# Kernel tuning notes

Measured on AMD Instinct MI355X. Metric: run time of the kernel, lower is better.

## Reference

```python
import jax, jax.numpy as jnp
import numpy as np

VOCAB = 32000
DIM = 1024
LAYERS = 4
B = 4
L = 1024


def setup_inputs() -> dict:
    key = jax.random.key(0)
    ks = jax.random.split(key, 5)
    input_ids = jax.random.randint(ks[0], (B, L), 0, VOCAB)
    embed = jax.random.normal(ks[1], (VOCAB, DIM), jnp.float32) * 0.02
    # 1/sqrt(fan_in) scaling keeps the recurrent state numerically stable over L steps
    W = jax.random.normal(ks[2], (LAYERS, 2 * DIM, 2 * DIM), jnp.float32) * (1.0 / np.sqrt(2 * DIM))
    out_w = jax.random.normal(ks[3], (VOCAB, DIM), jnp.float32) * 0.02
    starter = jax.random.normal(ks[4], (LAYERS, DIM), jnp.float32) * 0.02
    return {"input_ids": input_ids, "embed": embed, "W": W, "out_w": out_w, "starter": starter}


def reference(input_ids, embed, W, out_w, starter):
    Bsz, Lsz = input_ids.shape
    d = starter.shape[1]
    x = embed[input_ids]  # [B, L, d]
    # initial per-layer state, broadcast over batch: [layers, B, d]
    s0 = jnp.broadcast_to(starter[:, None, :], (W.shape[0], Bsz, d))

    def time_step(s_stack, x_t):
        # s_stack: [layers, B, d], x_t: [B, d]
        def layer_step(h, ws):
            Wi, si = ws  # Wi: [2d, 2d], si: [B, d]
            out = jnp.concatenate([h, si], axis=-1) @ Wi.T  # [B, 2d]
            h_new, s_new = jnp.split(out, 2, axis=-1)
            return h_new, s_new
        y, new_s = jax.lax.scan(layer_step, x_t, (W, s_stack))
        return new_s, y

    _, ys = jax.lax.scan(time_step, s0, jnp.swapaxes(x, 0, 1))  # ys: [L, B, d]
    logits = jnp.einsum('lbd,vd->blv', ys, out_w)  # [B, L, vocab]
    return logits
```

## Files before the change

kernel.cpp:

```cpp
#include <hip/hip_runtime.h>
#include <hip/hip_bf16.h>
#include <stdint.h>

#define BATCH 4
#define SEQ 1024
#define DIMX 1024
#define VOCAB 32000
#define NLAYERS 4
#define NBLK 256

#define W_GARR 4096
#define W_GREL 4608
#define W_LREL 4864
#define W_FLAG 5120

using bf16x8 = __attribute__((ext_vector_type(8))) short;
using f32x4v = __attribute__((ext_vector_type(4))) float;

__device__ __forceinline__ uint16_t f2b(float f) {
  __hip_bfloat16 h = __float2bfloat16(f);
  return *reinterpret_cast<uint16_t*>(&h);
}
__device__ __forceinline__ float b2f(uint16_t u) {
  __hip_bfloat16 h = *reinterpret_cast<__hip_bfloat16*>(&u);
  return __bfloat162float(h);
}
__device__ __forceinline__ void fsplit(float v, uint16_t& h, uint16_t& l) {
  h = f2b(v);
  l = f2b(v - b2f(h));
}

__device__ __forceinline__ uint32_t get_xcc() {
  uint32_t x;
  asm volatile("s_getreg_b32 %0, hwreg(HW_REG_XCC_ID)" : "=s"(x));
  return x & 7u;
}

__global__ __launch_bounds__(256) void k_embed_split(const int* __restrict__ ids,
                                                     const float* __restrict__ emb,
                                                     uint16_t* __restrict__ Hhi,
                                                     uint16_t* __restrict__ Hlo) {
  int idx = blockIdx.x * 256 + threadIdx.x;
  int d4 = idx & (DIMX / 4 - 1);
  int tb = idx >> 8;
  int t = tb >> 2, b = tb & 3;
  int id = ids[b * SEQ + t];
  float4 v = reinterpret_cast<const float4*>(emb + (size_t)id * DIMX)[d4];
  ushort4 h, l;
  fsplit(v.x, h.x, l.x); fsplit(v.y, h.y, l.y); fsplit(v.z, h.z, l.z); fsplit(v.w, h.w, l.w);
  reinterpret_cast<ushort4*>(Hhi)[idx] = h;
  reinterpret_cast<ushort4*>(Hlo)[idx] = l;
}

__global__ __launch_bounds__(256) void k_split_w(const float* __restrict__ W,
                                                 uint16_t* __restrict__ W1h, uint16_t* __restrict__ W1l,
                                                 uint16_t* __restrict__ WSh, uint16_t* __restrict__ WSl,
                                                 uint16_t* __restrict__ M1h, uint16_t* __restrict__ M1l) {
  int idx = blockIdx.x * 256 + threadIdx.x;
  int c4 = idx & 255;
  int row = idx >> 8;
  int l = row >> 12, r = row & 4095;
  const float* Wl = W + (size_t)l * 4 * 1024 * 1024;
  const float* src;
  uint16_t *dh, *dl;
  size_t doff;
  if (r < 2048) { src = Wl + (size_t)r * 2048; dh = W1h; dl = W1l; doff = ((size_t)l * 2048 + r) * 1024; }
  else if (r < 3072) { int rr = r - 2048; src = Wl + (size_t)rr * 2048 + 1024; dh = WSh; dl = WSl; doff = ((size_t)l * 1024 + rr) * 1024; }
  else { int rr = r - 3072; src = Wl + (size_t)(1024 + rr) * 2048 + 1024; dh = M1h; dl = M1l; doff = ((size_t)l * 1024 + rr) * 1024; }
  float4 v = reinterpret_cast<const float4*>(src)[c4];
  ushort4 h, lo4;
  fsplit(v.x, h.x, lo4.x); fsplit(v.y, h.y, lo4.y); fsplit(v.z, h.z, lo4.z); fsplit(v.w, h.w, lo4.w);
  reinterpret_cast<ushort4*>(dh + doff)[c4] = h;
  reinterpret_cast<ushort4*>(dl + doff)[c4] = lo4;
}

__global__ __launch_bounds__(256) void k_trans_w(const float* __restrict__ W,
                                                 uint16_t* __restrict__ T1h, uint16_t* __restrict__ T1l) {
  __shared__ float t[64][65];
  int l = blockIdx.z;
  const float* Wl = W + (size_t)l * 4 * 1024 * 1024;
  int i0 = blockIdx.y * 64, j0 = blockIdx.x * 64;
  int c4 = (threadIdx.x & 15) * 4, rr = threadIdx.x >> 4;
#pragma unroll
  for (int p = 0; p < 4; ++p) {
    int r = rr + p * 16;
    float4 v = *reinterpret_cast<const float4*>(Wl + (size_t)(1024 + i0 + r) * 2048 + 1024 + j0 + c4);
    t[r][c4] = v.x; t[r][c4 + 1] = v.y; t[r][c4 + 2] = v.z; t[r][c4 + 3] = v.w;
  }
  __syncthreads();
#pragma unroll
  for (int p = 0; p < 4; ++p) {
    int j = rr + p * 16;
    ushort4 h, l4;
    fsplit(t[c4 + 0][j], h.x, l4.x);
    fsplit(t[c4 + 1][j], h.y, l4.y);
    fsplit(t[c4 + 2][j], h.z, l4.z);
    fsplit(t[c4 + 3][j], h.w, l4.w);
    size_t o = (size_t)l * 1024 * 1024 + (size_t)(j0 + j) * 1024 + i0 + c4;
    *reinterpret_cast<ushort4*>(T1h + o) = h;
    *reinterpret_cast<ushort4*>(T1l + o) = l4;
  }
}

template <int BM, int BN>
__global__ __launch_bounds__(256) void k_mfma(
    int K,
    const uint16_t* __restrict__ Ahi, const uint16_t* __restrict__ Alo, int a_cs, int a_bs, size_t a_z,
    const uint16_t* __restrict__ Bhi, const uint16_t* __restrict__ Blo, int ldb, size_t b_z,
    const float* __restrict__ ADD, int add_cs, int add_bs,
    float* __restrict__ O1f, int o1_cs, int o1_bs,
    uint16_t* __restrict__ O1hi, uint16_t* __restrict__ O1lo, int o1s_cs, int o1s_bs, int split_n0, size_t o1_z,
    uint16_t* __restrict__ O2hi, uint16_t* __restrict__ O2lo, int o2_cs, int o2_bs, size_t o2_z) {
  constexpr int FM = BM / 32;
  constexpr int FN = BN / 32;
  __shared__ uint16_t sAh[BM * 32], sAl[BM * 32], sBh[BN * 32], sBl[BN * 32];
  size_t zb = blockIdx.z;
  Ahi += zb * a_z; Alo += zb * a_z;
  Bhi += zb * b_z; Blo += zb * b_z;
  if (O1hi) { O1hi += zb * o1_z; O1lo += zb * o1_z; }
  if (O2hi) { O2hi += zb * o2_z; O2lo += zb * o2_z; }
  int tid = threadIdx.x;
  int lane = tid & 63;
  int wave = tid >> 6;
  int wm = wave >> 1, wn = wave & 1;
  int m0 = blockIdx.y * BM, n0 = blockIdx.x * BN;
  f32x4v acc[FM][FN] = {};
  for (int kt = 0; kt < K; kt += 32) {
    __syncthreads();
#pragma unroll
    for (int q = 0; q < BM / 64; ++q) {
      int off = q * 4096 + tid * 16;
      int r = off >> 6;
      int cu = (off & 63) >> 1;
      size_t goff = (size_t)(m0 / 4 + (r >> 2)) * a_cs + (size_t)(r & 3) * a_bs + kt + cu;
      __builtin_amdgcn_global_load_lds(
          (const __attribute__((address_space(1))) uint32_t*)(Ahi + goff),
          (__attribute__((address_space(3))) uint32_t*)((char*)sAh + off), 16, 0, 0);
      __builtin_amdgcn_global_load_lds(
          (const __attribute__((address_space(1))) uint32_t*)(Alo + goff),
          (__attribute__((address_space(3))) uint32_t*)((char*)sAl + off), 16, 0, 0);
    }
#pragma unroll
    for (int q = 0; q < BN / 64; ++q) {
      int off = q * 4096 + tid * 16;
      int r = off >> 6, cu = (off & 63) >> 1;
      size_t goff = (size_t)(n0 + r) * ldb + kt + cu;
      __builtin_amdgcn_global_load_lds(
          (const __attribute__((address_space(1))) uint32_t*)(Bhi + goff),
          (__attribute__((address_space(3))) uint32_t*)((char*)sBh + off), 16, 0, 0);
      __builtin_amdgcn_global_load_lds(
          (const __attribute__((address_space(1))) uint32_t*)(Blo + goff),
          (__attribute__((address_space(3))) uint32_t*)((char*)sBl + off), 16, 0, 0);
    }
    __syncthreads();
    int rsel = lane & 15, ko = (lane >> 4) * 8;
    bf16x8 ah[FM], al[FM], bh[FN], bl[FN];
#pragma unroll
    for (int mf = 0; mf < FM; ++mf) {
      int row = wm * (FM * 16) + mf * 16 + rsel;
      ah[mf] = *reinterpret_cast<const bf16x8*>(sAh + row * 32 + ko);
      al[mf] = *reinterpret_cast<const bf16x8*>(sAl + row * 32 + ko);
    }
#pragma unroll
    for (int nf = 0; nf < FN; ++nf) {
      int row = wn * (FN * 16) + nf * 16 + rsel;
      bh[nf] = *reinterpret_cast<const bf16x8*>(sBh + row * 32 + ko);
      bl[nf] = *reinterpret_cast<const bf16x8*>(sBl + row * 32 + ko);
    }
#pragma unroll
    for (int mf = 0; mf < FM; ++mf)
#pragma unroll
      for (int nf = 0; nf < FN; ++nf) {
        acc[mf][nf] = __builtin_amdgcn_mfma_f32_16x16x32_bf16(ah[mf], bh[nf], acc[mf][nf], 0, 0, 0);
        acc[mf][nf] = __builtin_amdgcn_mfma_f32_16x16x32_bf16(ah[mf], bl[nf], acc[mf][nf], 0, 0, 0);
        acc[mf][nf] = __builtin_amdgcn_mfma_f32_16x16x32_bf16(al[mf], bh[nf], acc[mf][nf], 0, 0, 0);
      }
  }
  int rowg = (lane >> 4) * 4, colg = lane & 15;
#pragma unroll
  for (int mf = 0; mf < FM; ++mf)
#pragma unroll
    for (int nf = 0; nf < FN; ++nf)
#pragma unroll
      for (int r = 0; r < 4; ++r) {
        int m = m0 + wm * (FM * 16) + mf * 16 + rowg + r;
        int n = n0 + wn * (FN * 16) + nf * 16 + colg;
        size_t ro = (size_t)(m >> 2);
        float dot = acc[mf][nf][r];
        float v = dot;
        if (ADD) v += ADD[ro * add_cs + (size_t)(m & 3) * add_bs + n];
        if (O1f) O1f[ro * o1_cs + (size_t)(m & 3) * o1_bs + n] = v;
        if (O1hi && n >= split_n0) {
          uint16_t h, l;
          fsplit(v, h, l);
          size_t o = ro * o1s_cs + (size_t)(m & 3) * o1s_bs + (n - split_n0);
          O1hi[o] = h; O1lo[o] = l;
        }
        if (O2hi) {
          uint16_t h, l;
          fsplit(dot, h, l);
          size_t o = (o2_bs == 0) ? ((size_t)n * o2_cs + m)
                                  : (ro * o2_cs + (size_t)(m & 3) * o2_bs + n);
          O2hi[o] = h; O2lo[o] = l;
        }
      }
}

__device__ __forceinline__ void bar_any(uint32_t* S, int flat, int global, uint32_t& gen) {
  gen++;
  __syncthreads();
  int bid = blockIdx.x, tid = threadIdx.x;
  if (flat) {
    if (tid == 0)
      __hip_atomic_store(S + (size_t)bid * 16, gen, __ATOMIC_RELEASE, __HIP_MEMORY_SCOPE_AGENT);
    if (bid == 0) {
      while (__hip_atomic_load(S + (size_t)tid * 16, __ATOMIC_RELAXED, __HIP_MEMORY_SCOPE_AGENT) < gen)
        __builtin_amdgcn_s_sleep(2);
      __syncthreads();
      if (tid == 0) {
        __builtin_amdgcn_fence(__ATOMIC_ACQUIRE, "agent");
        __hip_atomic_store(S + W_GREL, gen, __ATOMIC_RELEASE, __HIP_MEMORY_SCOPE_AGENT);
      }
      __syncthreads();
    } else {
      if (tid == 0) {
        while (__hip_atomic_load(S + W_GREL, __ATOMIC_RELAXED, __HIP_MEMORY_SCOPE_AGENT) < gen)
          __builtin_amdgcn_s_sleep(2);
        __builtin_amdgcn_fence(__ATOMIC_ACQUIRE, "agent");
      }
      __syncthreads();
    }
    return;
  }
  int xcd = bid & 7, q = bid >> 3;
  if (global) {
    if (q != 0) {
      if (tid == 0) {
        __hip_atomic_store(S + (size_t)(xcd * 32 + q) * 16, gen, __ATOMIC_RELAXED, __HIP_MEMORY_SCOPE_AGENT);
        while (__hip_atomic_load(S + W_LREL + xcd * 16, __ATOMIC_RELAXED, __HIP_MEMORY_SCOPE_AGENT) < gen)
          __builtin_amdgcn_s_sleep(1);
        asm volatile("buffer_inv sc0" ::: "memory");
      }
      __builtin_amdgcn_sched_barrier(0);
      __syncthreads();
    } else {
      if (tid < 31) {
        uint32_t* s = S + (size_t)(xcd * 32 + 1 + tid) * 16;
        while (__hip_atomic_load(s, __ATOMIC_RELAXED, __HIP_MEMORY_SCOPE_AGENT) < gen)
          __builtin_amdgcn_s_sleep(1);
      }
      __syncthreads();
      if (tid == 0)
        __hip_atomic_store(S + W_GARR + xcd * 16, gen, __ATOMIC_RELEASE, __HIP_MEMORY_SCOPE_AGENT);
      if (xcd == 0) {
        if (tid < 8) {
          while (__hip_atomic_load(S + W_GARR + tid * 16, __ATOMIC_RELAXED, __HIP_MEMORY_SCOPE_AGENT) < gen)
            __builtin_amdgcn_s_sleep(1);
        }
        __syncthreads();
        if (tid == 0)
          __hip_atomic_store(S + W_GREL, gen, __ATOMIC_RELEASE, __HIP_MEMORY_SCOPE_AGENT);
      }
      if (tid == 0) {
        while (__hip_atomic_load(S + W_GREL, __ATOMIC_RELAXED, __HIP_MEMORY_SCOPE_AGENT) < gen)
          __builtin_amdgcn_s_sleep(1);
        __builtin_amdgcn_fence(__ATOMIC_ACQUIRE, "agent");
        __hip_atomic_store(S + W_LREL + xcd * 16, gen, __ATOMIC_RELEASE, __HIP_MEMORY_SCOPE_AGENT);
      }
      __builtin_amdgcn_sched_barrier(0);
      __syncthreads();
    }
  } else {
    if (q != 0) {
      if (tid == 0) {
        __hip_atomic_store(S + (size_t)(xcd * 32 + q) * 16, gen, __ATOMIC_RELAXED, __HIP_MEMORY_SCOPE_AGENT);
        while (__hip_atomic_load(S + W_LREL + xcd * 16, __ATOMIC_RELAXED, __HIP_MEMORY_SCOPE_AGENT) < gen)
          __builtin_amdgcn_s_sleep(1);
        asm volatile("buffer_inv sc0" ::: "memory");
      }
      __builtin_amdgcn_sched_barrier(0);
      __syncthreads();
    } else {
      if (tid < 31) {
        uint32_t* s = S + (size_t)(xcd * 32 + 1 + tid) * 16;
        while (__hip_atomic_load(s, __ATOMIC_RELAXED, __HIP_MEMORY_SCOPE_AGENT) < gen)
          __builtin_amdgcn_s_sleep(1);
      }
      __syncthreads();
      if (tid == 0) {
        asm volatile("buffer_inv sc0" ::: "memory");
        __hip_atomic_store(S + W_LREL + xcd * 16, gen, __ATOMIC_RELAXED, __HIP_MEMORY_SCOPE_AGENT);
      }
      __builtin_amdgcn_sched_barrier(0);
      __syncthreads();
    }
  }
}

__device__ __forceinline__ f32x4v wtile16(
    const uint16_t* __restrict__ Ah, const uint16_t* __restrict__ Al,
    int a_cs, int a_bs, int m0,
    const uint16_t* __restrict__ Bh, const uint16_t* __restrict__ Bl,
    int n0, int lane) {
  int rsel = lane & 15, ko = (lane >> 4) * 8;
  int am = m0 + rsel;
  const uint16_t* pah = Ah + (size_t)(am >> 2) * a_cs + (size_t)(am & 3) * a_bs + ko;
  const uint16_t* pal = Al + (size_t)(am >> 2) * a_cs + (size_t)(am & 3) * a_bs + ko;
  const uint16_t* pbh = Bh + (size_t)(n0 + rsel) * 1024 + ko;
  const uint16_t* pbl = Bl + (size_t)(n0 + rsel) * 1024 + ko;
  f32x4v acc = {0.f, 0.f, 0.f, 0.f};
#pragma unroll 4
  for (int kt = 0; kt < 1024; kt += 32) {
    bf16x8 ah = *reinterpret_cast<const bf16x8*>(pah + kt);
    bf16x8 al = *reinterpret_cast<const bf16x8*>(pal + kt);
    bf16x8 bh = *reinterpret_cast<const bf16x8*>(pbh + kt);
    bf16x8 bl = *reinterpret_cast<const bf16x8*>(pbl + kt);
    acc = __builtin_amdgcn_mfma_f32_16x16x32_bf16(ah, bh, acc, 0, 0, 0);
    acc = __builtin_amdgcn_mfma_f32_16x16x32_bf16(ah, bl, acc, 0, 0, 0);
    acc = __builtin_amdgcn_mfma_f32_16x16x32_bf16(al, bh, acc, 0, 0, 0);
  }
  return acc;
}

__device__ __forceinline__ f32x4v wtile16_lds(
    const uint16_t* __restrict__ Ah, const uint16_t* __restrict__ Al,
    int a_cs, int a_bs, int m0,
    const uint16_t* sBh, const uint16_t* sBl,
    int lane) {
  int rsel = lane & 15, ko = (lane >> 4) * 8;
  int am = m0 + rsel;
  const uint16_t* pah = Ah + (size_t)(am >> 2) * a_cs + (size_t)(am & 3) * a_bs + ko;
  const uint16_t* pal = Al + (size_t)(am >> 2) * a_cs + (size_t)(am & 3) * a_bs + ko;
  int rb = rsel * 1024;
  int s7 = rsel & 7;
  f32x4v acc0 = {0.f, 0.f, 0.f, 0.f}, acc1 = {0.f, 0.f, 0.f, 0.f};
#pragma unroll 4
  for (int kt = 0; kt < 1024; kt += 64) {
    int e0 = kt + ko, e1 = kt + 32 + ko;
    int o0 = rb + ((((e0) >> 3) ^ s7) << 3);
    int o1 = rb + ((((e1) >> 3) ^ s7) << 3);
    bf16x8 ah0 = *reinterpret_cast<const bf16x8*>(pah + kt);
    bf16x8 al0 = *reinterpret_cast<const bf16x8*>(pal + kt);
    bf16x8 ah1 = *reinterpret_cast<const bf16x8*>(pah + kt + 32);
    bf16x8 al1 = *reinterpret_cast<const bf16x8*>(pal + kt + 32);
    bf16x8 bh0 = *reinterpret_cast<const bf16x8*>(sBh + o0);
    bf16x8 bl0 = *reinterpret_cast<const bf16x8*>(sBl + o0);
    bf16x8 bh1 = *reinterpret_cast<const bf16x8*>(sBh + o1);
    bf16x8 bl1 = *reinterpret_cast<const bf16x8*>(sBl + o1);
    acc0 = __builtin_amdgcn_mfma_f32_16x16x32_bf16(ah0, bh0, acc0, 0, 0, 0);
    acc1 = __builtin_amdgcn_mfma_f32_16x16x32_bf16(ah1, bh1, acc1, 0, 0, 0);
    acc0 = __builtin_amdgcn_mfma_f32_16x16x32_bf16(ah0, bl0, acc0, 0, 0, 0);
    acc1 = __builtin_amdgcn_mfma_f32_16x16x32_bf16(ah1, bl1, acc1, 0, 0, 0);
    acc0 = __builtin_amdgcn_mfma_f32_16x16x32_bf16(al0, bh0, acc0, 0, 0, 0);
    acc1 = __builtin_amdgcn_mfma_f32_16x16x32_bf16(al1, bh1, acc1, 0, 0, 0);
  }
  return acc0 + acc1;
}

__global__ __launch_bounds__(256) void k_layer(
    uint32_t* S,
    float* __restrict__ P,
    uint16_t* __restrict__ PUh, uint16_t* __restrict__ PUl,
    uint16_t* __restrict__ Sh, uint16_t* __restrict__ Sl,
    const uint16_t* __restrict__ M1h, const uint16_t* __restrict__ M1l,
    const uint16_t* __restrict__ M16h, const uint16_t* __restrict__ M16l,
    const uint16_t* __restrict__ M128h, const uint16_t* __restrict__ M128l,
    uint16_t* G3h0, uint16_t* G3l0, uint16_t* G3h1, uint16_t* G3l1,
    uint16_t* BEh, uint16_t* BEl,
    float* LAMf, uint16_t* LAMh, uint16_t* LAMl,
    uint16_t* GSh0, uint16_t* GSl0, uint16_t* GSh1, uint16_t* GSl1,
    const float* __restrict__ starterL) {
  __shared__ uint16_t sB[2][32 * 1024];
  int tid = threadIdx.x, bid = blockIdx.x;
  int lane = tid & 63;
  int wv = tid >> 6;
  int xcd = bid & 7;
  int q = bid >> 3;
  uint32_t gen = 0;
  int rowg = (lane >> 4) * 4, colg = lane & 15;

  int m0_13 = xcd * 32 + (wv & 1) * 16;
  int n0_13 = (2 * q + (wv >> 1)) * 16;
  int lrb13 = (wv >> 1) * 16 * 1024;
  int n0_2 = (q * 4 + wv) * 16;

  {
    int idx = bid * 256 + tid;
    if (idx < BATCH * DIMX) {
      int b = idx >> 10, d = idx & 1023;
      float v = starterL[d];
      uint16_t h, l;
      fsplit(v, h, l);
      size_t o = (size_t)b * 1024 + d;
      BEh[o] = h; BEl[o] = l;
      G3h0[o] = h; G3l0[o] = l;
      GSh0[o] = h; GSl0[o] = l;
      Sh[o] = h; Sl[o] = l;
    }
  }

  if (tid == 0 && get_xcc() != (uint32_t)xcd)
    __hip_atomic_store(S + W_FLAG, 1u, __ATOMIC_RELAXED, __HIP_MEMORY_SCOPE_AGENT);
  bar_any(S, 1, 1, gen);
  int flat = (int)__hip_atomic_load(S + W_FLAG, __ATOMIC_RELAXED, __HIP_MEMORY_SCOPE_AGENT);

  {
    const uint16_t* gh = M1h + (size_t)(32 * q) * 1024;
    const uint16_t* gl = M1l + (size_t)(32 * q) * 1024;
    for (int i = tid; i < 32 * 128; i += 256) {
      int r = i >> 7, c8 = i & 127;
      int dst = r * 1024 + ((c8 ^ (r & 7)) << 3);
      *reinterpret_cast<bf16x8*>(&sB[0][dst]) = *reinterpret_cast<const bf16x8*>(gh + (size_t)r * 1024 + c8 * 8);
      *reinterpret_cast<bf16x8*>(&sB[1][dst]) = *reinterpret_cast<const bf16x8*>(gl + (size_t)r * 1024 + c8 * 8);
    }
  }
  __syncthreads();

  for (int j = 1; j < 16; ++j) {
    {
      f32x4v acc = wtile16_lds(PUh + (size_t)(j - 1) * 4096, PUl + (size_t)(j - 1) * 4096,
                               65536, 1024, m0_13, &sB[0][lrb13], &sB[1][lrb13], lane);
      int n = n0_13 + colg;
#pragma unroll
      for (int rr = 0; rr < 4; ++rr) {
        int m = m0_13 + rowg + rr;
        int c = m >> 2, b = m & 3;
        size_t t = (size_t)(c * 16 + j);
        float* pu = P + (t * 4 + b) * 2048 + 1024 + n;
        float v = acc[rr] + *pu;
        *pu = v;
        uint16_t h, l;
        fsplit(v, h, l);
        size_t o = (t * 4 + b) * 1024 + n;
        PUh[o] = h; PUl[o] = l;
      }
    }
    bar_any(S, flat, 0, gen);
  }

  if (q == 0) {
    for (int i = tid; i < 4096; i += 256) {
      int b = i >> 10, d = i & 1023;
      float v = P[((size_t)(xcd * 128 + 15) * 4 + b) * 2048 + 1024 + d];
      size_t o = (size_t)xcd * 16384 + (size_t)b * 1024 + d;
      LAMf[o] = v;
      uint16_t h, l;
      fsplit(v, h, l);
      LAMh[o] = h; LAMl[o] = l;
    }
  }
  bar_any(S, flat, 0, gen);

  for (int j = 1; j < 8; ++j) {
    if (q < 16) {
      size_t abase = (size_t)(j - 1) * 131072 + (size_t)xcd * 16384;
      f32x4v acc = wtile16(LAMh + abase, LAMl + abase, 4096, 1024, 0, M16h, M16l, n0_2, lane);
      if (rowg == 0) {
        int n = n0_2 + colg;
#pragma unroll
        for (int rr = 0; rr < 4; ++rr) {
          int b = rr;
          int c = 8 * xcd + j;
          float e = P[((size_t)(c * 16 + 15) * 4 + b) * 2048 + 1024 + n];
          float v = acc[rr] + e;
          size_t o = (size_t)j * 131072 + (size_t)xcd * 16384 + (size_t)b * 1024 + n;
          LAMf[o] = v;
          uint16_t h, l;
          fsplit(v, h, l);
          LAMh[o] = h; LAMl[o] = l;
        }
      }
    }
    bar_any(S, flat, (j == 7) ? 1 : 0, gen);
  }

  for (int g = 0; g < 7; ++g) {
    if (xcd == 0 && q < 16) {
      f32x4v acc = wtile16(BEh + (size_t)g * 16384, BEl + (size_t)g * 16384,
                           4096, 1024, 0, M128h, M128l, n0_2, lane);
      if (rowg == 0) {
        int n = n0_2 + colg;
#pragma unroll
        for (int rr = 0; rr < 4; ++rr) {
          int b = rr;
          float v = acc[rr] + LAMf[(size_t)7 * 131072 + (size_t)g * 16384 + (size_t)b * 1024 + n];
          uint16_t h, l;
          fsplit(v, h, l);
          size_t ob = (size_t)(g + 1) * 16384 + (size_t)b * 1024 + n;
          BEh[ob] = h; BEl[ob] = l;
          int c = 8 * (g + 1);
          size_t o1 = (size_t)(c * 4 + b) * 1024 + n;
          G3h0[o1] = h; G3l0[o1] = l;
          size_t o2 = ((size_t)(c * 16) * 4 + b) * 1024 + n;
          Sh[o2] = h; Sl[o2] = l;
          GSh0[ob] = h; GSl0[ob] = l;
        }
      }
    }
    bar_any(S, flat, (g == 6) ? 1 : 0, gen);
  }

  int gsc = 0;
  for (int j = 1; j < 8; ++j) {
    uint16_t* gih = gsc ? GSh1 : GSh0;
    uint16_t* gil = gsc ? GSl1 : GSl0;
    uint16_t* goh = gsc ? GSh0 : GSh1;
    uint16_t* gol = gsc ? GSl0 : GSl1;
    if (q < 16) {
      size_t gbase = (size_t)xcd * 16384;
      f32x4v acc = wtile16(gih + gbase, gil + gbase, 4096, 1024, 0, M16h, M16l, n0_2, lane);
      if (rowg == 0) {
        int n = n0_2 + colg;
#pragma unroll
        for (int rr = 0; rr < 4; ++rr) {
          int b = rr;
          int c = 8 * xcd + j;
          float lam = LAMf[(size_t)(j - 1) * 131072 + (size_t)xcd * 16384 + (size_t)b * 1024 + n];
          float v = acc[rr] + lam;
          uint16_t h, l;
          fsplit(v, h, l);
          size_t o1 = (size_t)(c * 4 + b) * 1024 + n;
          G3h0[o1] = h; G3l0[o1] = l;
          size_t o2 = ((size_t)(c * 16) * 4 + b) * 1024 + n;
          Sh[o2] = h; Sl[o2] = l;
          uint16_t h2, l2;
          fsplit(acc[rr], h2, l2);
          goh[gbase + (size_t)b * 1024 + n] = h2;
          gol[gbase + (size_t)b * 1024 + n] = l2;
        }
      }
    }
    bar_any(S, flat, 0, gen);
    gsc ^= 1;
  }

  int g3 = 0;
  for (int j = 1; j < 16; ++j) {
    uint16_t* gih = g3 ? G3h1 : G3h0;
    uint16_t* gil = g3 ? G3l1 : G3l0;
    uint16_t* goh = g3 ? G3h0 : G3h1;
    uint16_t* gol = g3 ? G3l0 : G3l1;
    {
      f32x4v acc = wtile16_lds(gih, gil, 4096, 1024, m0_13, &sB[0][lrb13], &sB[1][lrb13], lane);
      int n = n0_13 + colg;
#pragma unroll
      for (int rr = 0; rr < 4; ++rr) {
        int m = m0_13 + rowg + rr;
        int c = m >> 2, b = m & 3;
        float u = P[((size_t)(c * 16 + j - 1) * 4 + b) * 2048 + 1024 + n];
        float v = acc[rr] + u;
        uint16_t h, l;
        fsplit(v, h, l);
        size_t o = ((size_t)(c * 16 + j) * 4 + b) * 1024 + n;
        Sh[o] = h; Sl[o] = l;
        uint16_t h2, l2;
        fsplit(acc[rr], h2, l2);
        goh[(size_t)m * 1024 + n] = h2;
        gol[(size_t)m * 1024 + n] = l2;
      }
    }
    if (j < 15) bar_any(S, flat, 0, gen);
    g3 ^= 1;
  }
}

__global__ __launch_bounds__(256) void k_reorder_hi(const uint16_t* __restrict__ Hhi, uint16_t* __restrict__ Y) {
  int idx = blockIdx.x * 256 + threadIdx.x;
  int d4 = idx & (DIMX / 4 - 1);
  int tb = idx >> 8;
  int t = tb >> 2, b = tb & 3;
  ushort4 v = reinterpret_cast<const ushort4*>(Hhi)[idx];
  reinterpret_cast<ushort4*>(Y + (size_t)(b * SEQ + t) * DIMX)[d4] = v;
}

__global__ __launch_bounds__(256) void k_cast_w(const float* __restrict__ src, uint16_t* __restrict__ dst, int n4) {
  int idx = blockIdx.x * 256 + threadIdx.x;
  if (idx >= n4) return;
  float4 v = reinterpret_cast<const float4*>(src)[idx];
  ushort4 o;
  o.x = f2b(v.x); o.y = f2b(v.y); o.z = f2b(v.z); o.w = f2b(v.w);
  reinterpret_cast<ushort4*>(dst)[idx] = o;
}

__global__ __launch_bounds__(256) void k_logits(const uint16_t* __restrict__ A,
                                                const uint16_t* __restrict__ Bt,
                                                float* __restrict__ C) {
  __shared__ uint16_t As[128 * 32];
  __shared__ uint16_t Bs[128 * 32];
  int tid = threadIdx.x;
  int bx = blockIdx.x, by = blockIdx.y;
  int lane = tid & 63, wave = tid >> 6;
  int wm = wave >> 1, wn = wave & 1;
  f32x4v acc[4][4] = {};
  const uint16_t* Ag = A + (size_t)by * 128 * 1024;
  const uint16_t* Bg = Bt + (size_t)bx * 128 * 1024;
  for (int kt = 0; kt < 1024; kt += 32) {
    __syncthreads();
#pragma unroll
    for (int q = 0; q < 2; ++q) {
      int off = q * 4096 + tid * 16;
      int r = off >> 6, cu = (off & 63) >> 1;
      __builtin_amdgcn_global_load_lds(
          (const __attribute__((address_space(1))) uint32_t*)(Ag + (size_t)r * 1024 + kt + cu),
          (__attribute__((address_space(3))) uint32_t*)((char*)As + off), 16, 0, 0);
      __builtin_amdgcn_global_load_lds(
          (const __attribute__((address_space(1))) uint32_t*)(Bg + (size_t)r * 1024 + kt + cu),
          (__attribute__((address_space(3))) uint32_t*)((char*)Bs + off), 16, 0, 0);
    }
    __syncthreads();
    int rsel = lane & 15, ko = (lane >> 4) * 8;
    bf16x8 af[4], bfr[4];
#pragma unroll
    for (int mf = 0; mf < 4; ++mf)
      af[mf] = *reinterpret_cast<const bf16x8*>(As + (wm * 64 + mf * 16 + rsel) * 32 + ko);
#pragma unroll
    for (int nf = 0; nf < 4; ++nf)
      bfr[nf] = *reinterpret_cast<const bf16x8*>(Bs + (wn * 64 + nf * 16 + rsel) * 32 + ko);
#pragma unroll
    for (int mf = 0; mf < 4; ++mf)
#pragma unroll
      for (int nf = 0; nf < 4; ++nf)
        acc[mf][nf] = __builtin_amdgcn_mfma_f32_16x16x32_bf16(af[mf], bfr[nf], acc[mf][nf], 0, 0, 0);
  }
  int rowg = (lane >> 4) * 4;
  int colg = lane & 15;
#pragma unroll
  for (int mf = 0; mf < 4; ++mf)
#pragma unroll
    for (int nf = 0; nf < 4; ++nf)
#pragma unroll
      for (int r = 0; r < 4; ++r) {
        int m = by * 128 + wm * 64 + mf * 16 + rowg + r;
        int n = bx * 128 + wn * 64 + nf * 16 + colg;
        C[(size_t)m * VOCAB + n] = acc[mf][nf][r];
      }
}

extern "C" void kernel_launch(void* const* d_in, const int* in_sizes, int n_in,
                              void* d_out, int out_size, void* d_ws, size_t ws_size,
                              hipStream_t stream) {
  const int* ids = (const int*)d_in[0];
  const float* emb = (const float*)d_in[1];
  const float* W = (const float*)d_in[2];
  const float* outw = (const float*)d_in[3];
  const float* starter = (const float*)d_in[4];
  float* out = (float*)d_out;

  char* wsb = (char*)d_ws;
  size_t off = 0;
  auto alloc = [&](size_t bytes) {
    void* p = wsb + off;
    off = (off + bytes + 255) & ~(size_t)255;
    return p;
  };
  const size_t TB = SEQ * BATCH;
  const size_t MB1 = (size_t)1024 * 1024;

  uint32_t* SYNC = (uint32_t*)alloc((size_t)NLAYERS * 8192 * 4);
  uint16_t* Hh[2] = {(uint16_t*)alloc(TB * DIMX * 2), (uint16_t*)alloc(TB * DIMX * 2)};
  uint16_t* Hl[2] = {(uint16_t*)alloc(TB * DIMX * 2), (uint16_t*)alloc(TB * DIMX * 2)};
  float* P = (float*)alloc(TB * 2 * DIMX * 4);
  uint16_t* PUh = (uint16_t*)alloc(TB * DIMX * 2);
  uint16_t* PUl = (uint16_t*)alloc(TB * DIMX * 2);
  uint16_t* Sh = (uint16_t*)alloc(TB * DIMX * 2);
  uint16_t* Sl = (uint16_t*)alloc(TB * DIMX * 2);
  uint16_t* W1h = (uint16_t*)alloc((size_t)NLAYERS * 2048 * 1024 * 2);
  uint16_t* W1l = (uint16_t*)alloc((size_t)NLAYERS * 2048 * 1024 * 2);
  uint16_t* WSh = (uint16_t*)alloc((size_t)NLAYERS * MB1 * 2);
  uint16_t* WSl = (uint16_t*)alloc((size_t)NLAYERS * MB1 * 2);
  uint16_t* M1h = (uint16_t*)alloc((size_t)NLAYERS * MB1 * 2);
  uint16_t* M1l = (uint16_t*)alloc((size_t)NLAYERS * MB1 * 2);
  uint16_t* T1h = (uint16_t*)alloc((size_t)NLAYERS * MB1 * 2);
  uint16_t* T1l = (uint16_t*)alloc((size_t)NLAYERS * MB1 * 2);
  uint16_t* M16Ah = (uint16_t*)alloc((size_t)NLAYERS * MB1 * 2);
  uint16_t* M16Al = (uint16_t*)alloc((size_t)NLAYERS * MB1 * 2);
  uint16_t* M128Ah = (uint16_t*)alloc((size_t)NLAYERS * MB1 * 2);
  uint16_t* M128Al = (uint16_t*)alloc((size_t)NLAYERS * MB1 * 2);
  uint16_t* G3h0 = (uint16_t*)alloc((size_t)256 * 1024 * 2);
  uint16_t* G3l0 = (uint16_t*)alloc((size_t)256 * 1024 * 2);
  uint16_t* G3h1 = (uint16_t*)alloc((size_t)256 * 1024 * 2);
  uint16_t* G3l1 = (uint16_t*)alloc((size_t)256 * 1024 * 2);
  uint16_t* BEh = (uint16_t*)alloc((size_t)8 * 16 * 1024 * 2);
  uint16_t* BEl = (uint16_t*)alloc((size_t)8 * 16 * 1024 * 2);
  float* LAMf = (float*)alloc((size_t)8 * 128 * 1024 * 4);
  uint16_t* LAMh = (uint16_t*)alloc((size_t)8 * 128 * 1024 * 2);
  uint16_t* LAMl = (uint16_t*)alloc((size_t)8 * 128 * 1024 * 2);
  uint16_t* GSh0 = (uint16_t*)alloc((size_t)128 * 1024 * 2);
  uint16_t* GSl0 = (uint16_t*)alloc((size_t)128 * 1024 * 2);
  uint16_t* GSh1 = (uint16_t*)alloc((size_t)128 * 1024 * 2);
  uint16_t* GSl1 = (uint16_t*)alloc((size_t)128 * 1024 * 2);
  uint16_t* YSB = (uint16_t*)alloc(TB * DIMX * 2);
  uint16_t* OWB = (uint16_t*)alloc((size_t)VOCAB * DIMX * 2);

  uint16_t* CMh[2] = {(uint16_t*)P, Sh};
  uint16_t* CMl[2] = {(uint16_t*)P + 4 * MB1, Sl};
  uint16_t* CTh[2] = {(uint16_t*)P + 8 * MB1, Hh[1]};
  uint16_t* CTl[2] = {(uint16_t*)P + 12 * MB1, Hl[1]};

  hipMemsetAsync(SYNC, 0, (size_t)NLAYERS * 8192 * 4, stream);
  k_split_w<<<NLAYERS * 4096, 256, 0, stream>>>(W, W1h, W1l, WSh, WSl, M1h, M1l);
  k_trans_w<<<dim3(16, 16, NLAYERS), 256, 0, stream>>>(W, T1h, T1l);
  k_cast_w<<<(int)((size_t)VOCAB * DIMX / 4 / 256), 256, 0, stream>>>(outw, OWB, VOCAB * DIMX / 4);
  k_embed_split<<<(int)(TB * DIMX / 4 / 256), 256, 0, stream>>>(ids, emb, Hh[0], Hl[0]);

  {
    const uint16_t *inMh = M1h, *inMl = M1l, *inTh = T1h, *inTl = T1l;
    for (int k = 1; k <= 7; ++k) {
      uint16_t *oMh, *oMl;
      if (k == 4) { oMh = M16Ah; oMl = M16Al; }
      else if (k == 7) { oMh = M128Ah; oMl = M128Al; }
      else { oMh = CMh[k & 1]; oMl = CMl[k & 1]; }
      uint16_t* oTh = (k < 7) ? CTh[k & 1] : nullptr;
      uint16_t* oTl = (k < 7) ? CTl[k & 1] : nullptr;
      k_mfma<128, 128><<<dim3(8, 8, NLAYERS), 256, 0, stream>>>(
          1024,
          inMh, inMl, 4096, 1024, MB1,
          inTh, inTl, 1024, MB1,
          nullptr, 0, 0,
          nullptr, 0, 0,
          oMh, oMl, 4096, 1024, 0, MB1,
          oTh, oTl, 1024, 0, MB1);
      inMh = oMh; inMl = oMl; inTh = oTh; inTl = oTl;
    }
  }

  int cur = 0;
  for (int l = 0; l < NLAYERS; ++l) {
    k_mfma<128, 128><<<dim3(16, 32, 1), 256, 0, stream>>>(
        1024,
        Hh[cur], Hl[cur], 4096, 1024, 0,
        W1h + (size_t)l * 2048 * 1024, W1l + (size_t)l * 2048 * 1024, 1024, 0,
        nullptr, 0, 0,
        P, 8192, 2048,
        PUh, PUl, 4096, 1024, 1024, 0,
        nullptr, nullptr, 0, 1, 0);

    k_layer<<<NBLK, 256, 0, stream>>>(
        SYNC + (size_t)l * 8192,
        P, PUh, PUl, Sh, Sl,
        M1h + (size_t)l * MB1, M1l + (size_t)l * MB1,
        M16Ah + (size_t)l * MB1, M16Al + (size_t)l * MB1,
        M128Ah + (size_t)l * MB1, M128Al + (size_t)l * MB1,
        G3h0, G3l0, G3h1, G3l1,
        BEh, BEl, LAMf, LAMh, LAMl,
        GSh0, GSl0, GSh1, GSl1,
        starter + (size_t)l * DIMX);

    k_mfma<128, 128><<<dim3(8, 32, 1), 256, 0, stream>>>(
        1024,
        Sh, Sl, 4096, 1024, 0,
        WSh + (size_t)l * MB1, WSl + (size_t)l * MB1, 1024, 0,
        P, 8192, 2048,
        nullptr, 0, 0,
        Hh[cur ^ 1], Hl[cur ^ 1], 4096, 1024, 0, 0,
        nullptr, nullptr, 0, 1, 0);
    cur ^= 1;
  }

  k_reorder_hi<<<(int)(TB * DIMX / 4 / 256), 256, 0, stream>>>(Hh[cur], YSB);
  k_logits<<<dim3(VOCAB / 128, TB / 128), 256, 0, stream>>>(YSB, OWB, out);
}
```

Baseline: 4.206 ms.

## Replace sequential chunk scans with a log-depth tree reduction over matrix powers

Within each layer kernel, the per-chunk linear recurrence used to be solved with long sequential loops of grid barriers over 16-step chunks. It is now solved with a parallel-prefix tree that combines adjacent pairs using precomputed power matrices M^(2^k), with the precompute chain extended to nine squarings. This cuts the number of dependent barrier-separated steps per layer. In exchange it adds more GEMM work, more precomputed matrices and extra scratch buffers, and the tree combination order could change accumulated rounding in the hi/lo bf16 scheme.

```diff
diff --git a/kernel.cpp b/kernel.cpp
--- a/kernel.cpp
+++ b/kernel.cpp
@@ -17,6 +17,8 @@
 using bf16x8 = __attribute__((ext_vector_type(8))) short;
 using f32x4v = __attribute__((ext_vector_type(4))) float;
 
+#define MFMA __builtin_amdgcn_mfma_f32_16x16x32_bf16
+
 __device__ __forceinline__ uint16_t f2b(float f) {
   __hip_bfloat16 h = __float2bfloat16(f);
   return *reinterpret_cast<uint16_t*>(&h);
@@ -29,7 +31,6 @@
   h = f2b(v);
   l = f2b(v - b2f(h));
 }
-
 __device__ __forceinline__ uint32_t get_xcc() {
   uint32_t x;
   asm volatile("s_getreg_b32 %0, hwreg(HW_REG_XCC_ID)" : "=s"(x));
@@ -128,8 +129,8 @@
   for (int kt = 0; kt < K; kt += 32) {
     __syncthreads();
 #pragma unroll
-    for (int q = 0; q < BM / 64; ++q) {
-      int off = q * 4096 + tid * 16;
+    for (int qq = 0; qq < BM / 64; ++qq) {
+      int off = qq * 4096 + tid * 16;
       int r = off >> 6;
       int cu = (off & 63) >> 1;
       size_t goff = (size_t)(m0 / 4 + (r >> 2)) * a_cs + (size_t)(r & 3) * a_bs + kt + cu;
@@ -141,8 +142,8 @@
           (__attribute__((address_space(3))) uint32_t*)((char*)sAl + off), 16, 0, 0);
     }
 #pragma unroll
-    for (int q = 0; q < BN / 64; ++q) {
-      int off = q * 4096 + tid * 16;
+    for (int qq = 0; qq < BN / 64; ++qq) {
+      int off = qq * 4096 + tid * 16;
       int r = off >> 6, cu = (off & 63) >> 1;
       size_t goff = (size_t)(n0 + r) * ldb + kt + cu;
       __builtin_amdgcn_global_load_lds(
@@ -171,9 +172,9 @@
     for (int mf = 0; mf < FM; ++mf)
 #pragma unroll
       for (int nf = 0; nf < FN; ++nf) {
-        acc[mf][nf] = __builtin_amdgcn_mfma_f32_16x16x32_bf16(ah[mf], bh[nf], acc[mf][nf], 0, 0, 0);
-        acc[mf][nf] = __builtin_amdgcn_mfma_f32_16x16x32_bf16(ah[mf], bl[nf], acc[mf][nf], 0, 0, 0);
-        acc[mf][nf] = __builtin_amdgcn_mfma_f32_16x16x32_bf16(al[mf], bh[nf], acc[mf][nf], 0, 0, 0);
+        acc[mf][nf] = MFMA(ah[mf], bh[nf], acc[mf][nf], 0, 0, 0);
+        acc[mf][nf] = MFMA(ah[mf], bl[nf], acc[mf][nf], 0, 0, 0);
+        acc[mf][nf] = MFMA(al[mf], bh[nf], acc[mf][nf], 0, 0, 0);
       }
   }
   int rowg = (lane >> 4) * 4, colg = lane & 15;
@@ -206,7 +207,7 @@
       }
 }
 
-__device__ __forceinline__ void bar_any(uint32_t* S, int flat, int global, uint32_t& gen) {
+__device__ __forceinline__ void gbar(uint32_t* S, int flat, uint32_t& gen) {
   gen++;
   __syncthreads();
   int bid = blockIdx.x, tid = threadIdx.x;
@@ -233,334 +234,315 @@
     return;
   }
   int xcd = bid & 7, q = bid >> 3;
-  if (global) {
-    if (q != 0) {
-      if (tid == 0) {
-        __hip_atomic_store(S + (size_t)(xcd * 32 + q) * 16, gen, __ATOMIC_RELAXED, __HIP_MEMORY_SCOPE_AGENT);
-        while (__hip_atomic_load(S + W_LREL + xcd * 16, __ATOMIC_RELAXED, __HIP_MEMORY_SCOPE_AGENT) < gen)
-          __builtin_amdgcn_s_sleep(1);
-        asm volatile("buffer_inv sc0" ::: "memory");
-      }
-      __builtin_amdgcn_sched_barrier(0);
-      __syncthreads();
-    } else {
-      if (tid < 31) {
-        uint32_t* s = S + (size_t)(xcd * 32 + 1 + tid) * 16;
-        while (__hip_atomic_load(s, __ATOMIC_RELAXED, __HIP_MEMORY_SCOPE_AGENT) < gen)
+  if (q != 0) {
+    if (tid == 0) {
+      asm volatile("s_waitcnt vmcnt(0)" ::: "memory");
+      __hip_atomic_store(S + (size_t)(xcd * 32 + q) * 16, gen, __ATOMIC_RELAXED, __HIP_MEMORY_SCOPE_AGENT);
+      while (__hip_atomic_load(S + W_LREL + xcd * 16, __ATOMIC_RELAXED, __HIP_MEMORY_SCOPE_AGENT) < gen)
+        __builtin_amdgcn_s_sleep(1);
+      asm volatile("buffer_inv sc0" ::: "memory");
+    }
+    __builtin_amdgcn_sched_barrier(0);
+    __syncthreads();
+  } else {
+    if (tid < 31) {
+      uint32_t* s = S + (size_t)(xcd * 32 + 1 + tid) * 16;
+      while (__hip_atomic_load(s, __ATOMIC_RELAXED, __HIP_MEMORY_SCOPE_AGENT) < gen)
+        __builtin_amdgcn_s_sleep(1);
+    }
+    __syncthreads();
+    if (tid == 0)
+      __hip_atomic_store(S + W_GARR + xcd * 16, gen, __ATOMIC_RELEASE, __HIP_MEMORY_SCOPE_AGENT);
+    if (xcd == 0) {
+      if (tid < 8) {
+        while (__hip_atomic_load(S + W_GARR + tid * 16, __ATOMIC_RELAXED, __HIP_MEMORY_SCOPE_AGENT) < gen)
           __builtin_amdgcn_s_sleep(1);
       }
       __syncthreads();
       if (tid == 0)
-        __hip_atomic_store(S + W_GARR + xcd * 16, gen, __ATOMIC_RELEASE, __HIP_MEMORY_SCOPE_AGENT);
-      if (xcd == 0) {
-        if (tid < 8) {
-          while (__hip_atomic_load(S + W_GARR + tid * 16, __ATOMIC_RELAXED, __HIP_MEMORY_SCOPE_AGENT) < gen)
-            __builtin_amdgcn_s_sleep(1);
-        }
-        __syncthreads();
-        if (tid == 0)
-          __hip_atomic_store(S + W_GREL, gen, __ATOMIC_RELEASE, __HIP_MEMORY_SCOPE_AGENT);
-      }
-      if (tid == 0) {
-        while (__hip_atomic_load(S + W_GREL, __ATOMIC_RELAXED, __HIP_MEMORY_SCOPE_AGENT) < gen)
-          __builtin_amdgcn_s_sleep(1);
-        __builtin_amdgcn_fence(__ATOMIC_ACQUIRE, "agent");
-        __hip_atomic_store(S + W_LREL + xcd * 16, gen, __ATOMIC_RELEASE, __HIP_MEMORY_SCOPE_AGENT);
-      }
-      __builtin_amdgcn_sched_barrier(0);
-      __syncthreads();
-    }
-  } else {
-    if (q != 0) {
-      if (tid == 0) {
-        __hip_atomic_store(S + (size_t)(xcd * 32 + q) * 16, gen, __ATOMIC_RELAXED, __HIP_MEMORY_SCOPE_AGENT);
-        while (__hip_atomic_load(S + W_LREL + xcd * 16, __ATOMIC_RELAXED, __HIP_MEMORY_SCOPE_AGENT) < gen)
-          __builtin_amdgcn_s_sleep(1);
-        asm volatile("buffer_inv sc0" ::: "memory");
-      }
-      __builtin_amdgcn_sched_barrier(0);
-      __syncthreads();
-    } else {
-      if (tid < 31) {
-        uint32_t* s = S + (size_t)(xcd * 32 + 1 + tid) * 16;
-        while (__hip_atomic_load(s, __ATOMIC_RELAXED, __HIP_MEMORY_SCOPE_AGENT) < gen)
-          __builtin_amdgcn_s_sleep(1);
-      }
-      __syncthreads();
-      if (tid == 0) {
-        asm volatile("buffer_inv sc0" ::: "memory");
-        __hip_atomic_store(S + W_LREL + xcd * 16, gen, __ATOMIC_RELAXED, __HIP_MEMORY_SCOPE_AGENT);
-      }
-      __builtin_amdgcn_sched_barrier(0);
-      __syncthreads();
-    }
-  }
-}
-
-__device__ __forceinline__ f32x4v wtile16(
-    const uint16_t* __restrict__ Ah, const uint16_t* __restrict__ Al,
-    int a_cs, int a_bs, int m0,
-    const uint16_t* __restrict__ Bh, const uint16_t* __restrict__ Bl,
-    int n0, int lane) {
-  int rsel = lane & 15, ko = (lane >> 4) * 8;
-  int am = m0 + rsel;
-  const uint16_t* pah = Ah + (size_t)(am >> 2) * a_cs + (size_t)(am & 3) * a_bs + ko;
-  const uint16_t* pal = Al + (size_t)(am >> 2) * a_cs + (size_t)(am & 3) * a_bs + ko;
-  const uint16_t* pbh = Bh + (size_t)(n0 + rsel) * 1024 + ko;
-  const uint16_t* pbl = Bl + (size_t)(n0 + rsel) * 1024 + ko;
-  f32x4v acc = {0.f, 0.f, 0.f, 0.f};
+        __hip_atomic_store(S + W_GREL, gen, __ATOMIC_RELEASE, __HIP_MEMORY_SCOPE_AGENT);
+    }
+    if (tid == 0) {
+      while (__hip_atomic_load(S + W_GREL, __ATOMIC_RELAXED, __HIP_MEMORY_SCOPE_AGENT) < gen)
+        __builtin_amdgcn_s_sleep(1);
+      __builtin_amdgcn_fence(__ATOMIC_ACQUIRE, "agent");
+      __hip_atomic_store(S + W_LREL + xcd * 16, gen, __ATOMIC_RELEASE, __HIP_MEMORY_SCOPE_AGENT);
+    }
+    __builtin_amdgcn_sched_barrier(0);
+    __syncthreads();
+  }
+}
+
+__device__ __forceinline__ void wtile_dual(
+    const uint16_t* __restrict__ pah, const uint16_t* __restrict__ pal,
+    const uint16_t* sB0, const uint16_t* sB1,
+    int rsel, int ko, f32x4v& out0, f32x4v& out1) {
+  int s7 = rsel & 7;
+  int rb0 = rsel * 1024, rb1 = rb0 + 16 * 1024;
+  f32x4v a0 = {0.f, 0.f, 0.f, 0.f}, a1 = {0.f, 0.f, 0.f, 0.f};
 #pragma unroll 4
   for (int kt = 0; kt < 1024; kt += 32) {
+    int sw = ((((kt + ko) >> 3) ^ s7) << 3);
     bf16x8 ah = *reinterpret_cast<const bf16x8*>(pah + kt);
     bf16x8 al = *reinterpret_cast<const bf16x8*>(pal + kt);
-    bf16x8 bh = *reinterpret_cast<const bf16x8*>(pbh + kt);
-    bf16x8 bl = *reinterpret_cast<const bf16x8*>(pbl + kt);
-    acc = __builtin_amdgcn_mfma_f32_16x16x32_bf16(ah, bh, acc, 0, 0, 0);
-    acc = __builtin_amdgcn_mfma_f32_16x16x32_bf16(ah, bl, acc, 0, 0, 0);
-    acc = __builtin_amdgcn_mfma_f32_16x16x32_bf16(al, bh, acc, 0, 0, 0);
-  }
-  return acc;
-}
-
-__device__ __forceinline__ f32x4v wtile16_lds(
-    const uint16_t* __restrict__ Ah, const uint16_t* __restrict__ Al,
-    int a_cs, int a_bs, int m0,
-    const uint16_t* sBh, const uint16_t* sBl,
-    int lane) {
-  int rsel = lane & 15, ko = (lane >> 4) * 8;
-  int am = m0 + rsel;
-  const uint16_t* pah = Ah + (size_t)(am >> 2) * a_cs + (size_t)(am & 3) * a_bs + ko;
-  const uint16_t* pal = Al + (size_t)(am >> 2) * a_cs + (size_t)(am & 3) * a_bs + ko;
-  int rb = rsel * 1024;
-  int s7 = rsel & 7;
-  f32x4v acc0 = {0.f, 0.f, 0.f, 0.f}, acc1 = {0.f, 0.f, 0.f, 0.f};
-#pragma unroll 4
-  for (int kt = 0; kt < 1024; kt += 64) {
-    int e0 = kt + ko, e1 = kt + 32 + ko;
-    int o0 = rb + ((((e0) >> 3) ^ s7) << 3);
-    int o1 = rb + ((((e1) >> 3) ^ s7) << 3);
-    bf16x8 ah0 = *reinterpret_cast<const bf16x8*>(pah + kt);
-    bf16x8 al0 = *reinterpret_cast<const bf16x8*>(pal + kt);
-    bf16x8 ah1 = *reinterpret_cast<const bf16x8*>(pah + kt + 32);
-    bf16x8 al1 = *reinterpret_cast<const bf16x8*>(pal + kt + 32);
-    bf16x8 bh0 = *reinterpret_cast<const bf16x8*>(sBh + o0);
-    bf16x8 bl0 = *reinterpret_cast<const bf16x8*>(sBl + o0);
-    bf16x8 bh1 = *reinterpret_cast<const bf16x8*>(sBh + o1);
-    bf16x8 bl1 = *reinterpret_cast<const bf16x8*>(sBl + o1);
-    acc0 = __builtin_amdgcn_mfma_f32_16x16x32_bf16(ah0, bh0, acc0, 0, 0, 0);
-    acc1 = __builtin_amdgcn_mfma_f32_16x16x32_bf16(ah1, bh1, acc1, 0, 0, 0);
-    acc0 = __builtin_amdgcn_mfma_f32_16x16x32_bf16(ah0, bl0, acc0, 0, 0, 0);
-    acc1 = __builtin_amdgcn_mfma_f32_16x16x32_bf16(ah1, bl1, acc1, 0, 0, 0);
-    acc0 = __builtin_amdgcn_mfma_f32_16x16x32_bf16(al0, bh0, acc0, 0, 0, 0);
-    acc1 = __builtin_amdgcn_mfma_f32_16x16x32_bf16(al1, bh1, acc1, 0, 0, 0);
-  }
-  return acc0 + acc1;
+    bf16x8 b0h = *reinterpret_cast<const bf16x8*>(sB0 + rb0 + sw);
+    bf16x8 b0l = *reinterpret_cast<const bf16x8*>(sB1 + rb0 + sw);
+    bf16x8 b1h = *reinterpret_cast<const bf16x8*>(sB0 + rb1 + sw);
+    bf16x8 b1l = *reinterpret_cast<const bf16x8*>(sB1 + rb1 + sw);
+    a0 = MFMA(ah, b0h, a0, 0, 0, 0); a1 = MFMA(ah, b1h, a1, 0, 0, 0);
+    a0 = MFMA(ah, b0l, a0, 0, 0, 0); a1 = MFMA(ah, b1l, a1, 0, 0, 0);
+    a0 = MFMA(al, b0h, a0, 0, 0, 0); a1 = MFMA(al, b1h, a1, 0, 0, 0);
+  }
+  out0 = a0; out1 = a1;
 }
 
 __global__ __launch_bounds__(256) void k_layer(
     uint32_t* S,
-    float* __restrict__ P,
-    uint16_t* __restrict__ PUh, uint16_t* __restrict__ PUl,
+    const float* __restrict__ P,
+    const uint16_t* __restrict__ PUh, const uint16_t* __restrict__ PUl,
     uint16_t* __restrict__ Sh, uint16_t* __restrict__ Sl,
-    const uint16_t* __restrict__ M1h, const uint16_t* __restrict__ M1l,
-    const uint16_t* __restrict__ M16h, const uint16_t* __restrict__ M16l,
-    const uint16_t* __restrict__ M128h, const uint16_t* __restrict__ M128l,
-    uint16_t* G3h0, uint16_t* G3l0, uint16_t* G3h1, uint16_t* G3l1,
-    uint16_t* BEh, uint16_t* BEl,
-    float* LAMf, uint16_t* LAMh, uint16_t* LAMl,
-    uint16_t* GSh0, uint16_t* GSl0, uint16_t* GSh1, uint16_t* GSl1,
+    const uint16_t* __restrict__ MPh, const uint16_t* __restrict__ MPl, size_t mpk,
+    uint16_t* RAh, uint16_t* RAl, uint16_t* RBh, uint16_t* RBl,
+    uint16_t* Eah, uint16_t* Eal, uint16_t* Ebh, uint16_t* Ebl,
+    uint16_t* SIG0h, uint16_t* SIG0l,
+    uint16_t* Xbh, uint16_t* Xbl,
     const float* __restrict__ starterL) {
   __shared__ uint16_t sB[2][32 * 1024];
   int tid = threadIdx.x, bid = blockIdx.x;
-  int lane = tid & 63;
-  int wv = tid >> 6;
-  int xcd = bid & 7;
-  int q = bid >> 3;
+  int lane = tid & 63, wv = tid >> 6;
+  int xcd = bid & 7, q = bid >> 3;
+  int rsel = lane & 15, ko = (lane >> 4) * 8;
+  int rowg = (lane >> 4) * 4, colg = lane & 15;
+  int c0 = xcd * 8;
+  int nA = q * 32 + colg, nB = nA + 16;
   uint32_t gen = 0;
-  int rowg = (lane >> 4) * 4, colg = lane & 15;
-
-  int m0_13 = xcd * 32 + (wv & 1) * 16;
-  int n0_13 = (2 * q + (wv >> 1)) * 16;
-  int lrb13 = (wv >> 1) * 16 * 1024;
-  int n0_2 = (q * 4 + wv) * 16;
 
   {
     int idx = bid * 256 + tid;
-    if (idx < BATCH * DIMX) {
-      int b = idx >> 10, d = idx & 1023;
-      float v = starterL[d];
+    if (idx < 16 * 1024) {
+      int d = idx & 1023;
       uint16_t h, l;
-      fsplit(v, h, l);
-      size_t o = (size_t)b * 1024 + d;
-      BEh[o] = h; BEl[o] = l;
-      G3h0[o] = h; G3l0[o] = l;
-      GSh0[o] = h; GSl0[o] = l;
-      Sh[o] = h; Sl[o] = l;
+      fsplit(starterL[d], h, l);
+      SIG0h[idx] = h; SIG0l[idx] = l;
     }
   }
 
   if (tid == 0 && get_xcc() != (uint32_t)xcd)
     __hip_atomic_store(S + W_FLAG, 1u, __ATOMIC_RELAXED, __HIP_MEMORY_SCOPE_AGENT);
-  bar_any(S, 1, 1, gen);
+  gbar(S, 1, gen);
   int flat = (int)__hip_atomic_load(S + W_FLAG, __ATOMIC_RELAXED, __HIP_MEMORY_SCOPE_AGENT);
 
-  {
-    const uint16_t* gh = M1h + (size_t)(32 * q) * 1024;
-    const uint16_t* gl = M1l + (size_t)(32 * q) * 1024;
+  auto stage = [&](int k, int row0) {
+    const uint16_t* Bh = MPh + (size_t)k * mpk;
+    const uint16_t* Bl = MPl + (size_t)k * mpk;
     for (int i = tid; i < 32 * 128; i += 256) {
       int r = i >> 7, c8 = i & 127;
       int dst = r * 1024 + ((c8 ^ (r & 7)) << 3);
-      *reinterpret_cast<bf16x8*>(&sB[0][dst]) = *reinterpret_cast<const bf16x8*>(gh + (size_t)r * 1024 + c8 * 8);
-      *reinterpret_cast<bf16x8*>(&sB[1][dst]) = *reinterpret_cast<const bf16x8*>(gl + (size_t)r * 1024 + c8 * 8);
-    }
-  }
+      *reinterpret_cast<bf16x8*>(&sB[0][dst]) = *reinterpret_cast<const bf16x8*>(Bh + (size_t)(row0 + r) * 1024 + c8 * 8);
+      *reinterpret_cast<bf16x8*>(&sB[1][dst]) = *reinterpret_cast<const bf16x8*>(Bl + (size_t)(row0 + r) * 1024 + c8 * 8);
+    }
+  };
+
+  stage(0, q * 32);
   __syncthreads();
-
-  for (int j = 1; j < 16; ++j) {
-    {
-      f32x4v acc = wtile16_lds(PUh + (size_t)(j - 1) * 4096, PUl + (size_t)(j - 1) * 4096,
-                               65536, 1024, m0_13, &sB[0][lrb13], &sB[1][lrb13], lane);
-      int n = n0_13 + colg;
+  for (int mt = wv; mt < 16; mt += 4) {
+    int r = mt * 16 + rsel, b = r & 3, v = r >> 2;
+    int kk = v & 7, cl = v >> 3;
+    size_t ao = ((size_t)((c0 + cl) * 16 + 2 * kk) * 4 + b) * 1024 + ko;
+    f32x4v o0, o1;
+    wtile_dual(PUh + ao, PUl + ao, sB[0], sB[1], rsel, ko, o0, o1);
+#pragma unroll
+    for (int rr = 0; rr < 4; ++rr) {
+      int m = mt * 16 + rowg + rr, b2 = m & 3, v2 = m >> 2;
+      int k2 = v2 & 7, c2 = c0 + (v2 >> 3);
+      size_t po = ((size_t)(c2 * 16 + 2 * k2 + 1) * 4 + b2) * 2048 + 1024;
+      size_t oo = ((size_t)(c2 * 8 + k2) * 4 + b2) * 1024;
+      float v0 = o0[rr] + P[po + nA];
+      float v1 = o1[rr] + P[po + nB];
+      uint16_t h, l;
+      fsplit(v0, h, l); RAh[oo + nA] = h; RAl[oo + nA] = l;
+      fsplit(v1, h, l); RAh[oo + nB] = h; RAl[oo + nB] = l;
+    }
+  }
+  gbar(S, flat, gen);
+
+  auto treeLevel = [&](int Bk, int nLlog, int mtN,
+                       const uint16_t* inH, const uint16_t* inL,
+                       uint16_t* outH, uint16_t* outL) {
+    stage(Bk, q * 32);
+    __syncthreads();
+    int nL = 1 << nLlog;
+    for (int mt = wv; mt < mtN; mt += 4) {
+      int r = mt * 16 + rsel, b = r & 3, v = r >> 2;
+      int kk = v & (nL - 1), cl = v >> nLlog;
+      size_t ao = ((size_t)((c0 + cl) * 8 + 2 * kk) * 4 + b) * 1024 + ko;
+      f32x4v o0, o1;
+      wtile_dual(inH + ao, inL + ao, sB[0], sB[1], rsel, ko, o0, o1);
 #pragma unroll
       for (int rr = 0; rr < 4; ++rr) {
-        int m = m0_13 + rowg + rr;
-        int c = m >> 2, b = m & 3;
-        size_t t = (size_t)(c * 16 + j);
-        float* pu = P + (t * 4 + b) * 2048 + 1024 + n;
-        float v = acc[rr] + *pu;
-        *pu = v;
+        int m = mt * 16 + rowg + rr, b2 = m & 3, v2 = m >> 2;
+        int k2 = v2 & (nL - 1), c2 = c0 + (v2 >> nLlog);
+        size_t po = ((size_t)(c2 * 8 + 2 * k2 + 1) * 4 + b2) * 1024;
+        size_t oo = ((size_t)(c2 * 8 + k2) * 4 + b2) * 1024;
+        float r0 = b2f(inH[po + nA]) + b2f(inL[po + nA]) + o0[rr];
+        float r1 = b2f(inH[po + nB]) + b2f(inL[po + nB]) + o1[rr];
         uint16_t h, l;
-        fsplit(v, h, l);
-        size_t o = (t * 4 + b) * 1024 + n;
-        PUh[o] = h; PUl[o] = l;
-      }
-    }
-    bar_any(S, flat, 0, gen);
-  }
-
-  if (q == 0) {
-    for (int i = tid; i < 4096; i += 256) {
-      int b = i >> 10, d = i & 1023;
-      float v = P[((size_t)(xcd * 128 + 15) * 4 + b) * 2048 + 1024 + d];
-      size_t o = (size_t)xcd * 16384 + (size_t)b * 1024 + d;
-      LAMf[o] = v;
+        fsplit(r0, h, l); outH[oo + nA] = h; outL[oo + nA] = l;
+        fsplit(r1, h, l); outH[oo + nB] = h; outL[oo + nB] = l;
+      }
+    }
+    gbar(S, flat, gen);
+  };
+  treeLevel(1, 2, 8, RAh, RAl, RBh, RBl);
+  treeLevel(2, 1, 4, RBh, RBl, RAh, RAl);
+
+  stage(3, q * 32);
+  __syncthreads();
+  for (int mt = wv; mt < 2; mt += 4) {
+    int r = mt * 16 + rsel, b = r & 3, v = r >> 2;
+    size_t ao = ((size_t)((c0 + v) * 8) * 4 + b) * 1024 + ko;
+    f32x4v o0, o1;
+    wtile_dual(RAh + ao, RAl + ao, sB[0], sB[1], rsel, ko, o0, o1);
+#pragma unroll
+    for (int rr = 0; rr < 4; ++rr) {
+      int m = mt * 16 + rowg + rr, b2 = m & 3, v2 = m >> 2;
+      int c2 = c0 + v2;
+      size_t po = ((size_t)(c2 * 8 + 1) * 4 + b2) * 1024;
+      size_t eo = ((size_t)(c2 * 4 + b2)) * 1024;
+      float r0 = b2f(RAh[po + nA]) + b2f(RAl[po + nA]) + o0[rr];
+      float r1 = b2f(RAh[po + nB]) + b2f(RAl[po + nB]) + o1[rr];
       uint16_t h, l;
-      fsplit(v, h, l);
-      LAMh[o] = h; LAMl[o] = l;
-    }
-  }
-  bar_any(S, flat, 0, gen);
-
-  for (int j = 1; j < 8; ++j) {
-    if (q < 16) {
-      size_t abase = (size_t)(j - 1) * 131072 + (size_t)xcd * 16384;
-      f32x4v acc = wtile16(LAMh + abase, LAMl + abase, 4096, 1024, 0, M16h, M16l, n0_2, lane);
-      if (rowg == 0) {
-        int n = n0_2 + colg;
+      fsplit(r0, h, l); Eah[eo + nA] = h; Eal[eo + nA] = l;
+      fsplit(r1, h, l); Eah[eo + nB] = h; Eal[eo + nB] = l;
+    }
+  }
+  gbar(S, flat, gen);
+
+  int nbase = (xcd * 4 + q) * 32;
+  int nAB = nbase + colg, nBB = nAB + 16;
+
+  if (q < 4) stage(4, nbase);
+  __syncthreads();
+  if (q < 4 && wv == 0) {
+    size_t ao = (size_t)rsel * 1024 + ko;
+    f32x4v o0, o1;
+    wtile_dual(SIG0h + ao, SIG0l + ao, sB[0], sB[1], rsel, ko, o0, o1);
+#pragma unroll
+    for (int rr = 0; rr < 4; ++rr) {
+      int m = rowg + rr, b2 = m & 3, cp = m >> 2;
+      if (cp == 0) {
+        size_t eo = (size_t)b2 * 1024;
+        float r0 = b2f(Eah[eo + nAB]) + b2f(Eal[eo + nAB]) + o0[rr];
+        float r1 = b2f(Eah[eo + nBB]) + b2f(Eal[eo + nBB]) + o1[rr];
+        uint16_t h, l;
+        fsplit(r0, h, l); Eah[eo + nAB] = h; Eal[eo + nAB] = l;
+        fsplit(r1, h, l); Eah[eo + nBB] = h; Eal[eo + nBB] = l;
+      }
+    }
+  }
+  gbar(S, flat, gen);
+
+  for (int s = 0; s < 6; ++s) {
+    int p = 1 << s;
+    const uint16_t* Eoh = (s & 1) ? Ebh : Eah;
+    const uint16_t* Eol = (s & 1) ? Ebl : Eal;
+    uint16_t* Enh = (s & 1) ? Eah : Ebh;
+    uint16_t* Enl = (s & 1) ? Eal : Ebl;
+    if (q < 4) stage(4 + s, nbase);
+    __syncthreads();
+    if (q < 4) {
+      for (int mt = wv; mt < 16; mt += 4) {
+        int r = mt * 16 + rsel, b = r & 3, c = r >> 2;
+        int cin = (c >= p) ? (c - p) : c;
+        size_t ao = ((size_t)(cin * 4 + b)) * 1024 + ko;
+        f32x4v o0, o1;
+        wtile_dual(Eoh + ao, Eol + ao, sB[0], sB[1], rsel, ko, o0, o1);
 #pragma unroll
         for (int rr = 0; rr < 4; ++rr) {
-          int b = rr;
-          int c = 8 * xcd + j;
-          float e = P[((size_t)(c * 16 + 15) * 4 + b) * 2048 + 1024 + n];
-          float v = acc[rr] + e;
-          size_t o = (size_t)j * 131072 + (size_t)xcd * 16384 + (size_t)b * 1024 + n;
-          LAMf[o] = v;
+          int m = mt * 16 + rowg + rr, b2 = m & 3, c2 = m >> 2;
+          size_t eo = ((size_t)(c2 * 4 + b2)) * 1024;
+          if (c2 >= p) {
+            float r0 = b2f(Eoh[eo + nAB]) + b2f(Eol[eo + nAB]) + o0[rr];
+            float r1 = b2f(Eoh[eo + nBB]) + b2f(Eol[eo + nBB]) + o1[rr];
+            uint16_t h, l;
+            fsplit(r0, h, l); Enh[eo + nAB] = h; Enl[eo + nAB] = l;
+            fsplit(r1, h, l); Enh[eo + nBB] = h; Enl[eo + nBB] = l;
+          } else {
+            Enh[eo + nAB] = Eoh[eo + nAB]; Enl[eo + nAB] = Eol[eo + nAB];
+            Enh[eo + nBB] = Eoh[eo + nBB]; Enl[eo + nBB] = Eol[eo + nBB];
+          }
+        }
+      }
+    }
+    gbar(S, flat, gen);
+  }
+
+  {
+    int xt = q * 256 + tid;
+    for (int u = xt; u < 128 * 1024; u += 8192) {
+      int tl = u >> 10, b = (u >> 8) & 3, d4 = u & 255;
+      int t = c0 * 16 + tl;
+      int j = tl & 15;
+      int c = c0 + (tl >> 4);
+      float4 val;
+      if (j == 0) {
+        if (c == 0) {
+          val = reinterpret_cast<const float4*>(starterL)[d4];
+        } else {
+          size_t eo = ((size_t)((c - 1) * 4 + b)) * 1024 + d4 * 4;
+          ushort4 hh = *reinterpret_cast<const ushort4*>(Eah + eo);
+          ushort4 ll = *reinterpret_cast<const ushort4*>(Eal + eo);
+          val.x = b2f(hh.x) + b2f(ll.x);
+          val.y = b2f(hh.y) + b2f(ll.y);
+          val.z = b2f(hh.z) + b2f(ll.z);
+          val.w = b2f(hh.w) + b2f(ll.w);
+        }
+      } else {
+        val = *reinterpret_cast<const float4*>(P + ((size_t)(t - 1) * 4 + b) * 2048 + 1024 + d4 * 4);
+      }
+      size_t xo = ((size_t)t * 4 + b) * 1024 + d4 * 4;
+      ushort4 h4, l4;
+      fsplit(val.x, h4.x, l4.x); fsplit(val.y, h4.y, l4.y);
+      fsplit(val.z, h4.z, l4.z); fsplit(val.w, h4.w, l4.w);
+      *reinterpret_cast<ushort4*>(Sh + xo) = h4;
+      *reinterpret_cast<ushort4*>(Sl + xo) = l4;
+    }
+  }
+  gbar(S, flat, gen);
+
+  for (int s = 0; s < 4; ++s) {
+    int p = 1 << s;
+    const uint16_t* Xoh = (s & 1) ? Xbh : Sh;
+    const uint16_t* Xol = (s & 1) ? Xbl : Sl;
+    uint16_t* Xnh = (s & 1) ? Sh : Xbh;
+    uint16_t* Xnl = (s & 1) ? Sl : Xbl;
+    stage(s, q * 32);
+    __syncthreads();
+    for (int mt = wv; mt < 32; mt += 4) {
+      int r = mt * 16 + rsel, b = r & 3, v = r >> 2;
+      int j = v & 15, cl = v >> 4;
+      int jin = (j >= p) ? (j - p) : j;
+      size_t ao = ((size_t)((c0 + cl) * 16 + jin) * 4 + b) * 1024 + ko;
+      f32x4v o0, o1;
+      wtile_dual(Xoh + ao, Xol + ao, sB[0], sB[1], rsel, ko, o0, o1);
+#pragma unroll
+      for (int rr = 0; rr < 4; ++rr) {
+        int m = mt * 16 + rowg + rr, b2 = m & 3, v2 = m >> 2;
+        int j2 = v2 & 15, cl2 = v2 >> 4;
+        size_t xo = ((size_t)((c0 + cl2) * 16 + j2) * 4 + b2) * 1024;
+        if (j2 >= p) {
+          float r0 = b2f(Xoh[xo + nA]) + b2f(Xol[xo + nA]) + o0[rr];
+          float r1 = b2f(Xoh[xo + nB]) + b2f(Xol[xo + nB]) + o1[rr];
           uint16_t h, l;
-          fsplit(v, h, l);
-          LAMh[o] = h; LAMl[o] = l;
+          fsplit(r0, h, l); Xnh[xo + nA] = h; Xnl[xo + nA] = l;
+          fsplit(r1, h, l); Xnh[xo + nB] = h; Xnl[xo + nB] = l;
+        } else {
+          Xnh[xo + nA] = Xoh[xo + nA]; Xnl[xo + nA] = Xol[xo + nA];
+          Xnh[xo + nB] = Xoh[xo + nB]; Xnl[xo + nB] = Xol[xo + nB];
         }
       }
     }
-    bar_any(S, flat, (j == 7) ? 1 : 0, gen);
-  }
-
-  for (int g = 0; g < 7; ++g) {
-    if (xcd == 0 && q < 16) {
-      f32x4v acc = wtile16(BEh + (size_t)g * 16384, BEl + (size_t)g * 16384,
-                           4096, 1024, 0, M128h, M128l, n0_2, lane);
-      if (rowg == 0) {
-        int n = n0_2 + colg;
-#pragma unroll
-        for (int rr = 0; rr < 4; ++rr) {
-          int b = rr;
-          float v = acc[rr] + LAMf[(size_t)7 * 131072 + (size_t)g * 16384 + (size_t)b * 1024 + n];
-          uint16_t h, l;
-          fsplit(v, h, l);
-          size_t ob = (size_t)(g + 1) * 16384 + (size_t)b * 1024 + n;
-          BEh[ob] = h; BEl[ob] = l;
-          int c = 8 * (g + 1);
-          size_t o1 = (size_t)(c * 4 + b) * 1024 + n;
-          G3h0[o1] = h; G3l0[o1] = l;
-          size_t o2 = ((size_t)(c * 16) * 4 + b) * 1024 + n;
-          Sh[o2] = h; Sl[o2] = l;
-          GSh0[ob] = h; GSl0[ob] = l;
-        }
-      }
-    }
-    bar_any(S, flat, (g == 6) ? 1 : 0, gen);
-  }
-
-  int gsc = 0;
-  for (int j = 1; j < 8; ++j) {
-    uint16_t* gih = gsc ? GSh1 : GSh0;
-    uint16_t* gil = gsc ? GSl1 : GSl0;
-    uint16_t* goh = gsc ? GSh0 : GSh1;
-    uint16_t* gol = gsc ? GSl0 : GSl1;
-    if (q < 16) {
-      size_t gbase = (size_t)xcd * 16384;
-      f32x4v acc = wtile16(gih + gbase, gil + gbase, 4096, 1024, 0, M16h, M16l, n0_2, lane);
-      if (rowg == 0) {
-        int n = n0_2 + colg;
-#pragma unroll
-        for (int rr = 0; rr < 4; ++rr) {
-          int b = rr;
-          int c = 8 * xcd + j;
-          float lam = LAMf[(size_t)(j - 1) * 131072 + (size_t)xcd * 16384 + (size_t)b * 1024 + n];
-          float v = acc[rr] + lam;
-          uint16_t h, l;
-          fsplit(v, h, l);
-          size_t o1 = (size_t)(c * 4 + b) * 1024 + n;
-          G3h0[o1] = h; G3l0[o1] = l;
-          size_t o2 = ((size_t)(c * 16) * 4 + b) * 1024 + n;
-          Sh[o2] = h; Sl[o2] = l;
-          uint16_t h2, l2;
-          fsplit(acc[rr], h2, l2);
-          goh[gbase + (size_t)b * 1024 + n] = h2;
-          gol[gbase + (size_t)b * 1024 + n] = l2;
-        }
-      }
-    }
-    bar_any(S, flat, 0, gen);
-    gsc ^= 1;
-  }
-
-  int g3 = 0;
-  for (int j = 1; j < 16; ++j) {
-    uint16_t* gih = g3 ? G3h1 : G3h0;
-    uint16_t* gil = g3 ? G3l1 : G3l0;
-    uint16_t* goh = g3 ? G3h0 : G3h1;
-    uint16_t* gol = g3 ? G3l0 : G3l1;
-    {
-      f32x4v acc = wtile16_lds(gih, gil, 4096, 1024, m0_13, &sB[0][lrb13], &sB[1][lrb13], lane);
-      int n = n0_13 + colg;
-#pragma unroll
-      for (int rr = 0; rr < 4; ++rr) {
-        int m = m0_13 + rowg + rr;
-        int c = m >> 2, b = m & 3;
-        float u = P[((size_t)(c * 16 + j - 1) * 4 + b) * 2048 + 1024 + n];
-        float v = acc[rr] + u;
-        uint16_t h, l;
-        fsplit(v, h, l);
-        size_t o = ((size_t)(c * 16 + j) * 4 + b) * 1024 + n;
-        Sh[o] = h; Sl[o] = l;
-        uint16_t h2, l2;
-        fsplit(acc[rr], h2, l2);
-        goh[(size_t)m * 1024 + n] = h2;
-        gol[(size_t)m * 1024 + n] = l2;
-      }
-    }
-    if (j < 15) bar_any(S, flat, 0, gen);
-    g3 ^= 1;
+    if (s < 3) gbar(S, flat, gen);
   }
 }
 
@@ -597,8 +579,8 @@
   for (int kt = 0; kt < 1024; kt += 32) {
     __syncthreads();
 #pragma unroll
-    for (int q = 0; q < 2; ++q) {
-      int off = q * 4096 + tid * 16;
+    for (int qq = 0; qq < 2; ++qq) {
+      int off = qq * 4096 + tid * 16;
       int r = off >> 6, cu = (off & 63) >> 1;
       __builtin_amdgcn_global_load_lds(
           (const __attribute__((address_space(1))) uint32_t*)(Ag + (size_t)r * 1024 + kt + cu),
@@ -620,7 +602,7 @@
     for (int mf = 0; mf < 4; ++mf)
 #pragma unroll
       for (int nf = 0; nf < 4; ++nf)
-        acc[mf][nf] = __builtin_amdgcn_mfma_f32_16x16x32_bf16(af[mf], bfr[nf], acc[mf][nf], 0, 0, 0);
+        acc[mf][nf] = MFMA(af[mf], bfr[nf], acc[mf][nf], 0, 0, 0);
   }
   int rowg = (lane >> 4) * 4;
   int colg = lane & 15;
@@ -668,50 +650,44 @@
   uint16_t* W1l = (uint16_t*)alloc((size_t)NLAYERS * 2048 * 1024 * 2);
   uint16_t* WSh = (uint16_t*)alloc((size_t)NLAYERS * MB1 * 2);
   uint16_t* WSl = (uint16_t*)alloc((size_t)NLAYERS * MB1 * 2);
-  uint16_t* M1h = (uint16_t*)alloc((size_t)NLAYERS * MB1 * 2);
-  uint16_t* M1l = (uint16_t*)alloc((size_t)NLAYERS * MB1 * 2);
   uint16_t* T1h = (uint16_t*)alloc((size_t)NLAYERS * MB1 * 2);
   uint16_t* T1l = (uint16_t*)alloc((size_t)NLAYERS * MB1 * 2);
-  uint16_t* M16Ah = (uint16_t*)alloc((size_t)NLAYERS * MB1 * 2);
-  uint16_t* M16Al = (uint16_t*)alloc((size_t)NLAYERS * MB1 * 2);
-  uint16_t* M128Ah = (uint16_t*)alloc((size_t)NLAYERS * MB1 * 2);
-  uint16_t* M128Al = (uint16_t*)alloc((size_t)NLAYERS * MB1 * 2);
-  uint16_t* G3h0 = (uint16_t*)alloc((size_t)256 * 1024 * 2);
-  uint16_t* G3l0 = (uint16_t*)alloc((size_t)256 * 1024 * 2);
-  uint16_t* G3h1 = (uint16_t*)alloc((size_t)256 * 1024 * 2);
-  uint16_t* G3l1 = (uint16_t*)alloc((size_t)256 * 1024 * 2);
-  uint16_t* BEh = (uint16_t*)alloc((size_t)8 * 16 * 1024 * 2);
-  uint16_t* BEl = (uint16_t*)alloc((size_t)8 * 16 * 1024 * 2);
-  float* LAMf = (float*)alloc((size_t)8 * 128 * 1024 * 4);
-  uint16_t* LAMh = (uint16_t*)alloc((size_t)8 * 128 * 1024 * 2);
-  uint16_t* LAMl = (uint16_t*)alloc((size_t)8 * 128 * 1024 * 2);
-  uint16_t* GSh0 = (uint16_t*)alloc((size_t)128 * 1024 * 2);
-  uint16_t* GSl0 = (uint16_t*)alloc((size_t)128 * 1024 * 2);
-  uint16_t* GSh1 = (uint16_t*)alloc((size_t)128 * 1024 * 2);
-  uint16_t* GSl1 = (uint16_t*)alloc((size_t)128 * 1024 * 2);
+  uint16_t* TPh[2] = {(uint16_t*)alloc((size_t)NLAYERS * MB1 * 2), (uint16_t*)alloc((size_t)NLAYERS * MB1 * 2)};
+  uint16_t* TPl[2] = {(uint16_t*)alloc((size_t)NLAYERS * MB1 * 2), (uint16_t*)alloc((size_t)NLAYERS * MB1 * 2)};
+  uint16_t* MPh = (uint16_t*)alloc((size_t)10 * NLAYERS * MB1 * 2);
+  uint16_t* MPl = (uint16_t*)alloc((size_t)10 * NLAYERS * MB1 * 2);
+  uint16_t* RAh = (uint16_t*)alloc((size_t)64 * 8 * 4 * 1024 * 2);
+  uint16_t* RAl = (uint16_t*)alloc((size_t)64 * 8 * 4 * 1024 * 2);
+  uint16_t* RBh = (uint16_t*)alloc((size_t)64 * 8 * 4 * 1024 * 2);
+  uint16_t* RBl = (uint16_t*)alloc((size_t)64 * 8 * 4 * 1024 * 2);
+  uint16_t* Eah = (uint16_t*)alloc((size_t)64 * 4 * 1024 * 2);
+  uint16_t* Eal = (uint16_t*)alloc((size_t)64 * 4 * 1024 * 2);
+  uint16_t* Ebh = (uint16_t*)alloc((size_t)64 * 4 * 1024 * 2);
+  uint16_t* Ebl = (uint16_t*)alloc((size_t)64 * 4 * 1024 * 2);
+  uint16_t* SIG0h = (uint16_t*)alloc((size_t)16 * 1024 * 2);
+  uint16_t* SIG0l = (uint16_t*)alloc((size_t)16 * 1024 * 2);
+  uint16_t* Xbh = (uint16_t*)alloc(TB * DIMX * 2);
+  uint16_t* Xbl = (uint16_t*)alloc(TB * DIMX * 2);
   uint16_t* YSB = (uint16_t*)alloc(TB * DIMX * 2);
   uint16_t* OWB = (uint16_t*)alloc((size_t)VOCAB * DIMX * 2);
 
-  uint16_t* CMh[2] = {(uint16_t*)P, Sh};
-  uint16_t* CMl[2] = {(uint16_t*)P + 4 * MB1, Sl};
-  uint16_t* CTh[2] = {(uint16_t*)P + 8 * MB1, Hh[1]};
-  uint16_t* CTl[2] = {(uint16_t*)P + 12 * MB1, Hl[1]};
-
   hipMemsetAsync(SYNC, 0, (size_t)NLAYERS * 8192 * 4, stream);
-  k_split_w<<<NLAYERS * 4096, 256, 0, stream>>>(W, W1h, W1l, WSh, WSl, M1h, M1l);
+  k_split_w<<<NLAYERS * 4096, 256, 0, stream>>>(W, W1h, W1l, WSh, WSl, MPh, MPl);
   k_trans_w<<<dim3(16, 16, NLAYERS), 256, 0, stream>>>(W, T1h, T1l);
   k_cast_w<<<(int)((size_t)VOCAB * DIMX / 4 / 256), 256, 0, stream>>>(outw, OWB, VOCAB * DIMX / 4);
   k_embed_split<<<(int)(TB * DIMX / 4 / 256), 256, 0, stream>>>(ids, emb, Hh[0], Hl[0]);
 
   {
-    const uint16_t *inMh = M1h, *inMl = M1l, *inTh = T1h, *inTl = T1l;
-    for (int k = 1; k <= 7; ++k) {
-      uint16_t *oMh, *oMl;
-      if (k == 4) { oMh = M16Ah; oMl = M16Al; }
-      else if (k == 7) { oMh = M128Ah; oMl = M128Al; }
-      else { oMh = CMh[k & 1]; oMl = CMl[k & 1]; }
-      uint16_t* oTh = (k < 7) ? CTh[k & 1] : nullptr;
-      uint16_t* oTl = (k < 7) ? CTl[k & 1] : nullptr;
+    const size_t kstr = (size_t)NLAYERS * MB1;
+    for (int k = 1; k <= 9; ++k) {
+      const uint16_t* inMh = MPh + (size_t)(k - 1) * kstr;
+      const uint16_t* inMl = MPl + (size_t)(k - 1) * kstr;
+      const uint16_t* inTh = (k == 1) ? T1h : TPh[(k - 1) & 1];
+      const uint16_t* inTl = (k == 1) ? T1l : TPl[(k - 1) & 1];
+      uint16_t* oMh = MPh + (size_t)k * kstr;
+      uint16_t* oMl = MPl + (size_t)k * kstr;
+      uint16_t* oTh = (k <= 8) ? TPh[k & 1] : nullptr;
+      uint16_t* oTl = (k <= 8) ? TPl[k & 1] : nullptr;
       k_mfma<128, 128><<<dim3(8, 8, NLAYERS), 256, 0, stream>>>(
           1024,
           inMh, inMl, 4096, 1024, MB1,
@@ -720,7 +696,6 @@
           nullptr, 0, 0,
           oMh, oMl, 4096, 1024, 0, MB1,
           oTh, oTl, 1024, 0, MB1);
-      inMh = oMh; inMl = oMl; inTh = oTh; inTl = oTl;
     }
   }
 
@@ -738,12 +713,11 @@
     k_layer<<<NBLK, 256, 0, stream>>>(
         SYNC + (size_t)l * 8192,
         P, PUh, PUl, Sh, Sl,
-        M1h + (size_t)l * MB1, M1l + (size_t)l * MB1,
-        M16Ah + (size_t)l * MB1, M16Al + (size_t)l * MB1,
-        M128Ah + (size_t)l * MB1, M128Al + (size_t)l * MB1,
-        G3h0, G3l0, G3h1, G3l1,
-        BEh, BEl, LAMf, LAMh, LAMl,
-        GSh0, GSl0, GSh1, GSl1,
+        MPh + (size_t)l * MB1, MPl + (size_t)l * MB1, (size_t)NLAYERS * MB1,
+        RAh, RAl, RBh, RBl,
+        Eah, Eal, Ebh, Ebl,
+        SIG0h, SIG0l,
+        Xbh, Xbl,
         starter + (size_t)l * DIMX);
 
     k_mfma<128, 128><<<dim3(8, 32, 1), 256, 0, stream>>>(
```

Measured after the change: 5.609 ms. 33.4% more time.
